# Kernel tuning notes

Measured on AMD Instinct MI355X. Metric: run time of the kernel, lower is better.

Reference implementation:

```python
import jax, jax.numpy as jnp
import numpy as np

DEGREE = 3
NUM_KNOTS = 64


def make_knots(num_knots, degree):
    # concat(zeros(degree), linspace(0,1,K-degree+1), ones(degree)) -> len K+degree+1
    return jnp.concatenate([
        jnp.zeros(degree, dtype=jnp.float32),
        jnp.linspace(0.0, 1.0, num_knots - degree + 1, dtype=jnp.float32),
        jnp.ones(degree, dtype=jnp.float32),
    ])


def bspline_basis(x, knots, num_knots, degree):
    # Iterative Cox-de Boor DP, equivalent to the recursive basis_function.
    # x: [B, F] -> basis: [B, F, num_knots]
    t = knots
    xe = x[..., None]  # [B, F, 1]
    n0 = num_knots + degree
    i0 = jnp.arange(n0)
    # order-0: indicator t[i] <= x < t[i+1]
    B = ((t[i0] <= xe) & (xe < t[i0 + 1])).astype(x.dtype)  # [B, F, n0]
    for k in range(1, degree + 1):
        n = num_knots + degree - k
        i = jnp.arange(n)
        d1 = t[i + k] - t[i]
        d2 = t[i + k + 1] - t[i + 1]
        # terms are zero when the denominator is zero (clamped knots)
        w1 = jnp.where(d1 != 0, (xe - t[i]) / jnp.where(d1 != 0, d1, 1.0), 0.0)
        w2 = jnp.where(d2 != 0, (t[i + k + 1] - xe) / jnp.where(d2 != 0, d2, 1.0), 0.0)
        B = w1 * B[..., :n] + w2 * B[..., 1:n + 1]
    return B  # [B, F, num_knots]


def setup_inputs() -> dict:
    key = jax.random.key(0)
    k1, k2, k3 = jax.random.split(key, 3)
    x = jax.random.uniform(k1, (16384, 128), dtype=jnp.float32)  # x in [0,1)
    control_p = jax.random.normal(k2, (NUM_KNOTS, 128), dtype=jnp.float32)
    bias = jax.random.normal(k3, (128,), dtype=jnp.float32)
    return {"x": x, "control_p": control_p, "bias": bias}


def reference(x, control_p, bias):
    knots = make_knots(NUM_KNOTS, DEGREE)
    basis = bspline_basis(x, knots, NUM_KNOTS, DEGREE)  # [B, F, K]
    # torch: (basises.permute(1,2,0) * control_p).sum(dim=1) == einsum over K
    tout = jnp.einsum('bfk,kf->bf', basis, control_p)
    return tout + bias
```

## Files before the change

kernel.cpp:

```cpp
#include <hip/hip_runtime.h>

#define NUM_KNOTS 64
#define FEAT 128
#define NSEG 61

__device__ __forceinline__ float rcp_fast(float d) {
    return __builtin_amdgcn_rcpf(d);
}

__global__ __launch_bounds__(256, 4) void bspline_kernel(
    const float* __restrict__ x,
    const float* __restrict__ cp,
    const float* __restrict__ bias,
    float* __restrict__ out,
    int n)
{
    __shared__ float s_cp[NUM_KNOTS * FEAT];
    {
        const float4* cp4 = (const float4*)cp;
        float4* s4 = (float4*)s_cp;
        #pragma unroll
        for (int i = threadIdx.x; i < NUM_KNOTS * FEAT / 4; i += 256)
            s4[i] = cp4[i];
    }
    __syncthreads();

    const int tid0 = blockIdx.x * 256 + threadIdx.x;
    const int f = tid0 & (FEAT - 1);
    const float bv = bias[f];
    const float* col = s_cp + f;
    const int stride = gridDim.x * 256;

    for (int idx = tid0; idx < n; idx += stride) {
        float xx = x[idx];
        float y = xx * 61.0f;
        int j = (int)y;
        j = j > NSEG - 1 ? NSEG - 1 : j;

        float fj  = (float)j;
        float tm1 = (float)max(j - 1, 0);
        float tm2 = (float)max(j - 2, 0);
        float tp1 = fj + 1.0f;
        float tp2 = (float)min(j + 2, NSEG);
        float tp3 = (float)min(j + 3, NSEG);

        float l1 = y - fj, l2 = y - tm1, l3 = y - tm2;
        float r1 = tp1 - y, r2 = tp2 - y, r3 = tp3 - y;

        float N0 = r1, N1 = l1;
        float t0 = N0 * rcp_fast(tp1 - tm1);
        N0 = r1 * t0;
        float sv = l2 * t0;
        float t1 = N1 * rcp_fast(tp2 - fj);
        N1 = sv + r2 * t1;
        float N2 = l1 * t1;
        t0 = N0 * rcp_fast(tp1 - tm2);
        N0 = r1 * t0;
        sv = l3 * t0;
        t1 = N1 * rcp_fast(tp2 - tm1);
        N1 = sv + r2 * t1;
        sv = l2 * t1;
        float t2 = N2 * rcp_fast(tp3 - fj);
        N2 = sv + r3 * t2;
        float N3 = l1 * t2;

        float acc = N0 * col[j * FEAT]
                  + N1 * col[(j + 1) * FEAT]
                  + N2 * col[(j + 2) * FEAT]
                  + N3 * col[(j + 3) * FEAT];
        out[idx] = acc + bv;
    }
}

extern "C" void kernel_launch(void* const* d_in, const int* in_sizes, int n_in,
                              void* d_out, int out_size, void* d_ws, size_t ws_size,
                              hipStream_t stream) {
    const float* x    = (const float*)d_in[0];
    const float* cp   = (const float*)d_in[1];
    const float* bias = (const float*)d_in[2];
    float* out = (float*)d_out;
    int n = in_sizes[0];

    bspline_kernel<<<dim3(1024), dim3(256), 0, stream>>>(x, cp, bias, out, n);
}
```

Before: 68.25 us.

## Vectorize x/out as float4 and transpose control points in padded LDS

```diff
diff --git a/kernel.cpp b/kernel.cpp
--- a/kernel.cpp
+++ b/kernel.cpp
@@ -3,72 +3,96 @@
 #define NUM_KNOTS 64
 #define FEAT 128
 #define NSEG 61
+#define LDS_STRIDE 65
 
 __device__ __forceinline__ float rcp_fast(float d) {
     return __builtin_amdgcn_rcpf(d);
 }
 
+__device__ __forceinline__ float bspline_eval(float xx, const float* __restrict__ colT) {
+    float y = xx * 61.0f;
+    int j = (int)y;
+    j = j > NSEG - 1 ? NSEG - 1 : j;
+
+    float fj  = (float)j;
+    float tm1 = (float)max(j - 1, 0);
+    float tm2 = (float)max(j - 2, 0);
+    float tp1 = fj + 1.0f;
+    float tp2 = (float)min(j + 2, NSEG);
+    float tp3 = (float)min(j + 3, NSEG);
+
+    float l1 = y - fj, l2 = y - tm1, l3 = y - tm2;
+    float r1 = tp1 - y, r2 = tp2 - y, r3 = tp3 - y;
+
+    float N0 = r1, N1 = l1;
+    float t0 = N0 * rcp_fast(tp1 - tm1);
+    N0 = r1 * t0;
+    float sv = l2 * t0;
+    float t1 = N1 * rcp_fast(tp2 - fj);
+    N1 = sv + r2 * t1;
+    float N2 = l1 * t1;
+    t0 = N0 * rcp_fast(tp1 - tm2);
+    N0 = r1 * t0;
+    sv = l3 * t0;
+    t1 = N1 * rcp_fast(tp2 - tm1);
+    N1 = sv + r2 * t1;
+    sv = l2 * t1;
+    float t2 = N2 * rcp_fast(tp3 - fj);
+    N2 = sv + r3 * t2;
+    float N3 = l1 * t2;
+
+    const float* c = colT + j;
+    return N0 * c[0] + N1 * c[1] + N2 * c[2] + N3 * c[3];
+}
+
 __global__ __launch_bounds__(256, 4) void bspline_kernel(
-    const float* __restrict__ x,
-    const float* __restrict__ cp,
-    const float* __restrict__ bias,
-    float* __restrict__ out,
-    int n)
+    const float4* __restrict__ x4,
+    const float*  __restrict__ cp,
+    const float*  __restrict__ bias,
+    float4* __restrict__ out4,
+    int n4)
 {
-    __shared__ float s_cp[NUM_KNOTS * FEAT];
-    {
-        const float4* cp4 = (const float4*)cp;
-        float4* s4 = (float4*)s_cp;
-        #pragma unroll
-        for (int i = threadIdx.x; i < NUM_KNOTS * FEAT / 4; i += 256)
-            s4[i] = cp4[i];
+    __shared__ float s_cpT[FEAT * LDS_STRIDE];
+    for (int u = threadIdx.x; u < NUM_KNOTS * FEAT; u += 256) {
+        int f = u & (FEAT - 1);
+        int k = u >> 7;
+        s_cpT[f * LDS_STRIDE + k] = cp[u];
     }
     __syncthreads();
 
-    const int tid0 = blockIdx.x * 256 + threadIdx.x;
-    const int f = tid0 & (FEAT - 1);
-    const float bv = bias[f];
-    const float* col = s_cp + f;
+    const int tid = blockIdx.x * 256 + threadIdx.x;
     const int stride = gridDim.x * 256;
+    const int f0 = (tid * 4) & (FEAT - 1);
+    const float4 bv = *(const float4*)(bias + f0);
+    const float* c0 = s_cpT + f0 * LDS_STRIDE;
+    const float* c1 = c0 + LDS_STRIDE;
+    const float* c2 = c1 + LDS_STRIDE;
+    const float* c3 = c2 + LDS_STRIDE;
 
-    for (int idx = tid0; idx < n; idx += stride) {
-        float xx = x[idx];
-        float y = xx * 61.0f;
-        int j = (int)y;
-        j = j > NSEG - 1 ? NSEG - 1 : j;
-
-        float fj  = (float)j;
-        float tm1 = (float)max(j - 1, 0);
-        float tm2 = (float)max(j - 2, 0);
-        float tp1 = fj + 1.0f;
-        float tp2 = (float)min(j + 2, NSEG);
-        float tp3 = (float)min(j + 3, NSEG);
-
-        float l1 = y - fj, l2 = y - tm1, l3 = y - tm2;
-        float r1 = tp1 - y, r2 = tp2 - y, r3 = tp3 - y;
-
-        float N0 = r1, N1 = l1;
-        float t0 = N0 * rcp_fast(tp1 - tm1);
-        N0 = r1 * t0;
-        float sv = l2 * t0;
-        float t1 = N1 * rcp_fast(tp2 - fj);
-        N1 = sv + r2 * t1;
-        float N2 = l1 * t1;
-        t0 = N0 * rcp_fast(tp1 - tm2);
-        N0 = r1 * t0;
-        sv = l3 * t0;
-        t1 = N1 * rcp_fast(tp2 - tm1);
-        N1 = sv + r2 * t1;
-        sv = l2 * t1;
-        float t2 = N2 * rcp_fast(tp3 - fj);
-        N2 = sv + r3 * t2;
-        float N3 = l1 * t2;
-
-        float acc = N0 * col[j * FEAT]
-                  + N1 * col[(j + 1) * FEAT]
-                  + N2 * col[(j + 2) * FEAT]
-                  + N3 * col[(j + 3) * FEAT];
-        out[idx] = acc + bv;
+    int i = tid;
+    for (; i + stride < n4; i += 2 * stride) {
+        float4 xa = x4[i];
+        float4 xb = x4[i + stride];
+        float4 oa, ob;
+        oa.x = bspline_eval(xa.x, c0) + bv.x;
+        oa.y = bspline_eval(xa.y, c1) + bv.y;
+        oa.z = bspline_eval(xa.z, c2) + bv.z;
+        oa.w = bspline_eval(xa.w, c3) + bv.w;
+        ob.x = bspline_eval(xb.x, c0) + bv.x;
+        ob.y = bspline_eval(xb.y, c1) + bv.y;
+        ob.z = bspline_eval(xb.z, c2) + bv.z;
+        ob.w = bspline_eval(xb.w, c3) + bv.w;
+        out4[i] = oa;
+        out4[i + stride] = ob;
+    }
+    for (; i < n4; i += stride) {
+        float4 xv = x4[i];
+        float4 ov;
+        ov.x = bspline_eval(xv.x, c0) + bv.x;
+        ov.y = bspline_eval(xv.y, c1) + bv.y;
+        ov.z = bspline_eval(xv.z, c2) + bv.z;
+        ov.w = bspline_eval(xv.w, c3) + bv.w;
+        out4[i] = ov;
     }
 }
 
@@ -80,6 +104,8 @@
     const float* bias = (const float*)d_in[2];
     float* out = (float*)d_out;
     int n = in_sizes[0];
+    int n4 = n >> 2;
 
-    bspline_kernel<<<dim3(1024), dim3(256), 0, stream>>>(x, cp, bias, out, n);
+    bspline_kernel<<<dim3(1024), dim3(256), 0, stream>>>(
+        (const float4*)x, cp, bias, (float4*)out, n4);
 }
```

New measurement: 67.38 us. No clear change (-1.3%).
